# Kernel tuning notes

Measured on AMD Instinct MI355X. Metric: run time of the kernel, lower is better.

## Reference

```python
import jax, jax.numpy as jnp
import numpy as np

B, D, L = 32, 576, 196          # batch, literals per patch, patches
Cc, K = 10, 256                 # classes, clauses per class
M = Cc * K                      # total clauses
MASK_DENSITY = 0.02             # fraction of literals included per clause (sparse so clauses actually fire)


def setup_inputs() -> dict:
    key = jax.random.key(0)
    k1, k2, k3 = jax.random.split(key, 3)
    # literals in {0,1} as float (as produced by the upstream TMCNNClass binarizer)
    literals = jax.random.bernoulli(k1, 0.5, (B, D, L)).astype(jnp.float32)
    # sparse clause selection masks [M, D]
    clause_mask = jax.random.uniform(k2, (M, D)) < MASK_DENSITY
    # per-clause vote weights alpha [M]
    alpha = jax.random.normal(k3, (M,), dtype=jnp.float32)
    return {"literals": literals, "clause_mask": clause_mask, "alpha": alpha}


def reference(literals, clause_mask, alpha):
    # Original: lit_masked = where(mask, lit, 1); clause_map = lit_masked.min(dim=D) == 1.
    # With literals in {0,1} this AND-reduce equals: no selected literal is 0, i.e.
    # sum over selected literals of (1 - lit) == 0. Expressed as a GEMM to avoid
    # materializing the B*M*D*L broadcast intermediate.
    mask_f = clause_mask.astype(literals.dtype)                 # [M, D]
    miss = jnp.einsum('md,bdl->bml', mask_f, 1.0 - literals)    # [B, M, L] count of violated literals
    clause_map = miss < 0.5                                     # exact ==0 test on small nonneg ints
    clause_or = jnp.any(clause_map, axis=-1)                    # [B, M] OR over patches

    # Weighted vote: first K/2 clauses per class are positive, second K/2 negative.
    z = clause_or.astype(literals.dtype).reshape(B, Cc, K)      # [B, Cc, K]
    h = K // 2
    sign = jnp.concatenate([jnp.ones((h,), literals.dtype), -jnp.ones((h,), literals.dtype)])
    logits = jnp.einsum('bck,ck->bc', z, alpha.reshape(Cc, K) * sign)  # [B, Cc]
    return clause_map, clause_or, logits
```

## Files before the change

kernel.cpp:

```cpp
#include <hip/hip_runtime.h>
#include <stdint.h>

#define B  32
#define D  576
#define L  196
#define CC 10
#define K  256
#define M  (CC * K)
#define SLOTS 64
#define NF4 49

#define PACK_BLOCKS ((B * D + 3) / 4)
#define CSR_BLOCKS  ((M + 3) / 4)

__global__ __launch_bounds__(256) void prologue_k(
    const float* __restrict__ lit, const int* __restrict__ mask,
    uint64_t* __restrict__ litbits, int* __restrict__ cnt,
    uint16_t* __restrict__ list) {
    const int lane = threadIdx.x & 63;
    const int wave = threadIdx.x >> 6;

    if (blockIdx.x < PACK_BLOCKS) {
        const int wid = blockIdx.x * 4 + wave;
        if (wid >= B * D) return;
        const int b = wid % B;
        const int d = wid / B;
        const float* base = lit + ((size_t)b * D + d) * L;

        uint64_t w0 = __ballot(base[lane] > 0.5f);
        uint64_t w1 = __ballot(base[64 + lane] > 0.5f);
        uint64_t w2 = __ballot(base[128 + lane] > 0.5f);
        float tail = (lane < 4) ? base[192 + lane] : 0.0f;
        uint64_t w3 = __ballot(tail > 0.5f);

        uint64_t* out = litbits + ((size_t)d * B + b) * 4;
        if (lane == 0) { out[0] = w0; out[1] = w1; out[2] = w2; out[3] = w3; }
    } else {
        const int m = (blockIdx.x - PACK_BLOCKS) * 4 + wave;
        if (m >= M) return;
        const int* row = mask + (size_t)m * D;
        int base = 0;
#pragma unroll
        for (int r = 0; r < 9; ++r) {
            int d = r * 64 + lane;
            bool sel = (row[d] != 0);
            uint64_t bal = __ballot(sel);
            if (sel) {
                int pos = base + __popcll(bal & ((1ull << lane) - 1ull));
                if (pos < SLOTS) list[(size_t)m * SLOTS + pos] = (uint16_t)d;
            }
            base += __popcll(bal);
        }
        if (lane == 0) cnt[m] = (base < SLOTS) ? base : SLOTS;
    }
}

__global__ __launch_bounds__(128) void clause_eval3_k(
    const uint64_t* __restrict__ litbits, const int* __restrict__ cnt,
    const uint16_t* __restrict__ list, float* __restrict__ cmap,
    float* __restrict__ cor) {
    __shared__ uint64_t res[64 * 4];
    __shared__ uint16_t sh_list[2 * SLOTS];

    const int t    = threadIdx.x;
    const int pair = t >> 1;
    const int h    = t & 1;
    const int b    = pair & 31;
    const int mm   = pair >> 5;
    const int m0   = blockIdx.x * 2;
    const int m    = m0 + mm;

    sh_list[t] = list[(size_t)(m0 + (t >> 6)) * SLOTS + (t & 63)];
    const int n = cnt[m];
    __syncthreads();

    uint64_t a0 = ~0ull, a1 = ~0ull;
    const uint16_t* lst = sh_list + mm * SLOTS;
    for (int k = 0; k < n; ++k) {
        int d = (int)lst[k];
        const ulonglong2 v =
            *(const ulonglong2*)(litbits + (((size_t)d * B + b) * 4 + 2 * h));
        a0 &= v.x;
        a1 &= v.y;
    }
    res[pair * 4 + 2 * h]     = a0;
    res[pair * 4 + 2 * h + 1] = a1;
    __syncthreads();

    for (int f = t; f < 64 * NF4; f += 128) {
        int r  = f / NF4;
        int q  = f - r * NF4;
        int wd = q >> 4;
        int sh = (q & 15) * 4;
        unsigned nib = (unsigned)((res[r * 4 + wd] >> sh) & 0xFull);
        float4 o;
        o.x = (nib & 1u) ? 1.0f : 0.0f;
        o.y = (nib & 2u) ? 1.0f : 0.0f;
        o.z = (nib & 4u) ? 1.0f : 0.0f;
        o.w = (nib & 8u) ? 1.0f : 0.0f;
        int bb = r & 31, mr = r >> 5;
        ((float4*)cmap)[((size_t)bb * M + m0 + mr) * NF4 + q] = o;
    }

    if (t < 64) {
        uint64_t w = res[t * 4] | res[t * 4 + 1] | res[t * 4 + 2] | res[t * 4 + 3];
        int bb = t & 31, mr = t >> 5;
        cor[(size_t)bb * M + m0 + mr] = w ? 1.0f : 0.0f;
    }
}

__global__ __launch_bounds__(256) void logits_k(
    const float* __restrict__ cor, const float* __restrict__ alpha,
    float* __restrict__ logits) {
    const int c = blockIdx.x % CC;
    const int b = blockIdx.x / CC;
    const int k = threadIdx.x;
    const float sgn = (k < (K / 2)) ? 1.0f : -1.0f;
    float v = cor[(size_t)b * M + (size_t)c * K + k] * alpha[(size_t)c * K + k] * sgn;
#pragma unroll
    for (int off = 32; off > 0; off >>= 1) v += __shfl_down(v, off, 64);
    __shared__ float sv[4];
    if ((k & 63) == 0) sv[k >> 6] = v;
    __syncthreads();
    if (k == 0) logits[blockIdx.x] = sv[0] + sv[1] + sv[2] + sv[3];
}

extern "C" void kernel_launch(void* const* d_in, const int* in_sizes, int n_in,
                              void* d_out, int out_size, void* d_ws, size_t ws_size,
                              hipStream_t stream) {
    const float* lit   = (const float*)d_in[0];
    const int*   mask  = (const int*)  d_in[1];
    const float* alpha = (const float*)d_in[2];

    float* out    = (float*)d_out;
    float* cmap   = out;
    float* cor    = out + (size_t)B * M * L;
    float* logits = cor + (size_t)B * M;

    uint64_t* litbits = (uint64_t*)d_ws;
    int*      cnt     = (int*)(litbits + (size_t)D * B * 4);
    uint16_t* list    = (uint16_t*)(cnt + M);

    prologue_k<<<PACK_BLOCKS + CSR_BLOCKS, 256, 0, stream>>>(
        lit, mask, litbits, cnt, list);

    clause_eval3_k<<<M / 2, 128, 0, stream>>>(litbits, cnt, list, cmap, cor);

    logits_k<<<B * CC, 256, 0, stream>>>(cor, alpha, logits);
}
```

Measured before the change: 99.69 us.

## Remap clause eval blocks to one batch row and 64 contiguous clauses

```diff
diff --git a/kernel.cpp b/kernel.cpp
--- a/kernel.cpp
+++ b/kernel.cpp
@@ -9,6 +9,7 @@
 #define M  (CC * K)
 #define SLOTS 64
 #define NF4 49
+#define MT 64
 
 #define PACK_BLOCKS ((B * D + 3) / 4)
 #define CSR_BLOCKS  ((M + 3) / 4)
@@ -55,57 +56,65 @@
     }
 }
 
-__global__ __launch_bounds__(128) void clause_eval3_k(
+__global__ __launch_bounds__(128) void clause_eval4_k(
     const uint64_t* __restrict__ litbits, const int* __restrict__ cnt,
     const uint16_t* __restrict__ list, float* __restrict__ cmap,
     float* __restrict__ cor) {
-    __shared__ uint64_t res[64 * 4];
-    __shared__ uint16_t sh_list[2 * SLOTS];
+    __shared__ uint64_t res[MT * 4];
+    __shared__ uint16_t sh_list[MT * SLOTS];
+    __shared__ int      sh_cnt[MT];
 
-    const int t    = threadIdx.x;
-    const int pair = t >> 1;
-    const int h    = t & 1;
-    const int b    = pair & 31;
-    const int mm   = pair >> 5;
-    const int m0   = blockIdx.x * 2;
-    const int m    = m0 + mm;
+    const int t  = threadIdx.x;
+    const int m0 = blockIdx.x * MT;
+    const int b  = blockIdx.y;
 
-    sh_list[t] = list[(size_t)(m0 + (t >> 6)) * SLOTS + (t & 63)];
-    const int n = cnt[m];
+    {
+        const uint4* lp = (const uint4*)(list + (size_t)m0 * SLOTS);
+        uint4* sp = (uint4*)sh_list;
+#pragma unroll
+        for (int i = t; i < MT * SLOTS * 2 / 16; i += 128) sp[i] = lp[i];
+        if (t < MT) sh_cnt[t] = cnt[m0 + t];
+    }
     __syncthreads();
 
-    uint64_t a0 = ~0ull, a1 = ~0ull;
-    const uint16_t* lst = sh_list + mm * SLOTS;
-    for (int k = 0; k < n; ++k) {
-        int d = (int)lst[k];
-        const ulonglong2 v =
-            *(const ulonglong2*)(litbits + (((size_t)d * B + b) * 4 + 2 * h));
-        a0 &= v.x;
-        a1 &= v.y;
+    {
+        const int c = t >> 1;
+        const int h = t & 1;
+        const int n = sh_cnt[c];
+        const uint16_t* lst = sh_list + c * SLOTS;
+        uint64_t a0 = ~0ull, a1 = ~0ull;
+        for (int k = 0; k < n; ++k) {
+            int d = (int)lst[k];
+            const ulonglong2 v =
+                *(const ulonglong2*)(litbits + (((size_t)d * B + b) * 4 + 2 * h));
+            a0 &= v.x;
+            a1 &= v.y;
+        }
+        res[c * 4 + 2 * h]     = a0;
+        res[c * 4 + 2 * h + 1] = a1;
     }
-    res[pair * 4 + 2 * h]     = a0;
-    res[pair * 4 + 2 * h + 1] = a1;
     __syncthreads();
 
-    for (int f = t; f < 64 * NF4; f += 128) {
-        int r  = f / NF4;
-        int q  = f - r * NF4;
-        int wd = q >> 4;
-        int sh = (q & 15) * 4;
-        unsigned nib = (unsigned)((res[r * 4 + wd] >> sh) & 0xFull);
-        float4 o;
-        o.x = (nib & 1u) ? 1.0f : 0.0f;
-        o.y = (nib & 2u) ? 1.0f : 0.0f;
-        o.z = (nib & 4u) ? 1.0f : 0.0f;
-        o.w = (nib & 8u) ? 1.0f : 0.0f;
-        int bb = r & 31, mr = r >> 5;
-        ((float4*)cmap)[((size_t)bb * M + m0 + mr) * NF4 + q] = o;
+    {
+        float4* outp = (float4*)cmap + ((size_t)b * M + m0) * NF4;
+        for (int f = t; f < MT * NF4; f += 128) {
+            int c  = f / NF4;
+            int q  = f - c * NF4;
+            int wd = q >> 4;
+            int sh = (q & 15) * 4;
+            unsigned nib = (unsigned)((res[c * 4 + wd] >> sh) & 0xFull);
+            float4 o;
+            o.x = (nib & 1u) ? 1.0f : 0.0f;
+            o.y = (nib & 2u) ? 1.0f : 0.0f;
+            o.z = (nib & 4u) ? 1.0f : 0.0f;
+            o.w = (nib & 8u) ? 1.0f : 0.0f;
+            outp[f] = o;
+        }
     }
 
-    if (t < 64) {
+    if (t < MT) {
         uint64_t w = res[t * 4] | res[t * 4 + 1] | res[t * 4 + 2] | res[t * 4 + 3];
-        int bb = t & 31, mr = t >> 5;
-        cor[(size_t)bb * M + m0 + mr] = w ? 1.0f : 0.0f;
+        cor[(size_t)b * M + m0 + t] = w ? 1.0f : 0.0f;
     }
 }
 
@@ -144,7 +153,8 @@
     prologue_k<<<PACK_BLOCKS + CSR_BLOCKS, 256, 0, stream>>>(
         lit, mask, litbits, cnt, list);
 
-    clause_eval3_k<<<M / 2, 128, 0, stream>>>(litbits, cnt, list, cmap, cor);
+    clause_eval4_k<<<dim3(M / MT, B), 128, 0, stream>>>(
+        litbits, cnt, list, cmap, cor);
 
     logits_k<<<B * CC, 256, 0, stream>>>(cor, alpha, logits);
 }
```

New measurement: 102.4 us. +2.7%, slower.
